# Kernel tuning notes

Measured on AMD Instinct MI355X. Metric: run time of the kernel, lower is better.

## Reference

```python
import jax, jax.numpy as jnp
import numpy as np

N = 20000
E = 320000
D = 512
H = 512


def _gcn_norm(edge_index, num_nodes):
    # PyG GCNConv: add self-loops, then sym-normalize with in-degree of A+I
    src = jnp.concatenate([edge_index[0], jnp.arange(num_nodes)])
    dst = jnp.concatenate([edge_index[1], jnp.arange(num_nodes)])
    deg = jax.ops.segment_sum(jnp.ones_like(dst, dtype=jnp.float32), dst, num_segments=num_nodes)
    dinv = jnp.where(deg > 0, jax.lax.rsqrt(deg), 0.0)
    norm = dinv[src] * dinv[dst]  # [E+N]
    return src, dst, norm


def _gcn_layer(x, src, dst, norm, W, b, num_nodes):
    h = x @ W                          # [N, out]
    msg = h[src] * norm[:, None]       # gather + scale, [E+N, out]
    out = jax.ops.segment_sum(msg, dst, num_segments=num_nodes)  # scatter-add
    return out + b


def setup_inputs() -> dict:
    key = jax.random.key(0)
    ks = jax.random.split(key, 8)
    features = jax.random.normal(ks[0], (N, D), dtype=jnp.float32)
    edge_index = jax.random.randint(ks[1], (2, E), 0, N, dtype=jnp.int64)
    edge_attr = jax.random.normal(ks[2], (E, 1), dtype=jnp.float32)  # unused by GCNConv
    s1 = 1.0 / np.sqrt(D)
    s2 = 1.0 / np.sqrt(H)
    W1 = jax.random.uniform(ks[3], (D, H), dtype=jnp.float32, minval=-s1, maxval=s1)
    b1 = jnp.zeros((H,), dtype=jnp.float32)
    W2 = jax.random.uniform(ks[4], (H, H), dtype=jnp.float32, minval=-s2, maxval=s2)
    b2 = jnp.zeros((H,), dtype=jnp.float32)
    return {"features": features, "edge_index": edge_index, "edge_attr": edge_attr,
            "W1": W1, "b1": b1, "W2": W2, "b2": b2}


def reference(features, edge_index, edge_attr, W1, b1, W2, b2):
    src, dst, norm = _gcn_norm(edge_index, N)
    x = jax.nn.relu(_gcn_layer(features, src, dst, norm, W1, b1, N))
    x = jax.nn.relu(_gcn_layer(x, src, dst, norm, W2, b2, N))
    # global_max_pool over the single graph (batch = all zeros) -> [1, H]
    return jnp.max(x, axis=0, keepdims=True)
```

## Files before the change

### kernel.cpp

```cpp
#include <hip/hip_runtime.h>

#define N_NODES 20000
#define MP      20096
#define N_EDGES 320000
#define DIM     512
#define SCAN_BLOCKS 79
#define FILL_BLOCKS 1250
#define CVT_BLOCKS  2512
#define W_BLOCKS    512
#define SORT_BLOCKS 79
#define NBIN 4096
#define MAXP_BLOCKS 256
#define MAXP_ROWS   79

typedef _Float16 half8 __attribute__((ext_vector_type(8)));
typedef _Float16 half4v __attribute__((ext_vector_type(4)));
typedef float floatx4 __attribute__((ext_vector_type(4)));

#define GLD16(g, l) __builtin_amdgcn_global_load_lds( \
    (const __attribute__((address_space(1))) unsigned int*)(g), \
    (__attribute__((address_space(3))) unsigned int*)(l), 16, 0, 0)

__global__ void k_count(const int* __restrict__ dst, int* __restrict__ cnt) {
    int e = blockIdx.x * blockDim.x + threadIdx.x;
    if (e < N_EDGES) atomicAdd(&cnt[dst[e]], 1);
}

__global__ __launch_bounds__(256) void k_scan_a(const int* __restrict__ cnt,
                                                int* __restrict__ bsum) {
    __shared__ int buf[256];
    int gi = blockIdx.x * 256 + threadIdx.x;
    buf[threadIdx.x] = (gi < N_NODES) ? cnt[gi] : 0;
    __syncthreads();
    for (int off = 128; off > 0; off >>= 1) {
        if (threadIdx.x < off) buf[threadIdx.x] += buf[threadIdx.x + off];
        __syncthreads();
    }
    if (threadIdx.x == 0) bsum[blockIdx.x] = buf[0];
}

__global__ __launch_bounds__(128) void k_scan_b(const int* __restrict__ bsum,
                                                int* __restrict__ bbase) {
    __shared__ int buf[128];
    int tid = threadIdx.x;
    int v = (tid < SCAN_BLOCKS) ? bsum[tid] : 0;
    buf[tid] = v;
    __syncthreads();
    for (int off = 1; off < 128; off <<= 1) {
        int t = (tid >= off) ? buf[tid - off] : 0;
        __syncthreads();
        buf[tid] += t;
        __syncthreads();
    }
    if (tid < SCAN_BLOCKS) bbase[tid] = buf[tid] - v;
}

__global__ __launch_bounds__(256) void k_scan_c(const int* __restrict__ cnt,
                                                const int* __restrict__ bbase,
                                                int* __restrict__ offs,
                                                int* __restrict__ cursor,
                                                float* __restrict__ dinv,
                                                int* __restrict__ hist) {
    __shared__ int buf[256];
    __shared__ int lh[NBIN];
    int tid = threadIdx.x;
#pragma unroll
    for (int k = 0; k < NBIN / 256; ++k) lh[tid + k * 256] = 0;
    int gi = blockIdx.x * 256 + tid;
    int v = (gi < N_NODES) ? cnt[gi] : 0;
    buf[tid] = v;
    __syncthreads();
    for (int off = 1; off < 256; off <<= 1) {
        int t = (tid >= off) ? buf[tid - off] : 0;
        __syncthreads();
        buf[tid] += t;
        __syncthreads();
    }
    int base = bbase[blockIdx.x];
    if (gi < N_NODES) {
        int incl = base + buf[tid];
        offs[gi + 1] = incl;
        cursor[gi] = incl - v;
        dinv[gi] = rsqrtf((float)v + 1.0f);
        if (gi == 0) offs[0] = 0;
        int bin = (v > 255 ? 255 : v) * 16 + (gi & 15);
        atomicAdd(&lh[bin], 1);
    } else if (gi < MP) {
        dinv[gi] = 0.f;
    }
    __syncthreads();
#pragma unroll
    for (int k = 0; k < NBIN / 256; ++k) {
        int b2 = tid + k * 256;
        if (lh[b2]) atomicAdd(&hist[b2], lh[b2]);
    }
}

__global__ __launch_bounds__(256) void k_prep(const int* __restrict__ src,
                                              const int* __restrict__ dst,
                                              int* __restrict__ cursor,
                                              int* __restrict__ csr_src,
                                              const float* __restrict__ F,
                                              _Float16* __restrict__ A,
                                              const float* __restrict__ W1,
                                              const float* __restrict__ W2,
                                              _Float16* __restrict__ Wt1,
                                              _Float16* __restrict__ Wt2,
                                              const int* __restrict__ cnt,
                                              const int* __restrict__ hist,
                                              int* __restrict__ bincur,
                                              int* __restrict__ sorted) {
    int b = blockIdx.x;
    if (b < FILL_BLOCKS) {
        int e = b * 256 + threadIdx.x;
        int d = dst[e];
        int pos = atomicAdd(&cursor[d], 1);
        csr_src[pos] = src[e];
        return;
    }
    if (b < FILL_BLOCKS + CVT_BLOCKS) {
        int base = (b - FILL_BLOCKS) * 1024 + threadIdx.x;
#pragma unroll
        for (int k = 0; k < 4; ++k) {
            int i = base + k * 256;
            int e = i * 4;
            int row = e >> 9;
            half4v o;
            if (row < N_NODES) {
                float4 v = *(const float4*)&F[e];
                o[0] = (_Float16)v.x; o[1] = (_Float16)v.y;
                o[2] = (_Float16)v.z; o[3] = (_Float16)v.w;
            } else {
                o[0] = o[1] = o[2] = o[3] = (_Float16)0.f;
            }
            *(half4v*)&A[e] = o;
        }
        return;
    }
    if (b < FILL_BLOCKS + CVT_BLOCKS + W_BLOCKS) {
        int local = b - (FILL_BLOCKS + CVT_BLOCKS);
        int z = local >> 8, t = local & 255;
        const float* W = z ? W2 : W1;
        _Float16* Wt = z ? Wt2 : Wt1;
        __shared__ float tile[32][33];
        int bx = (t & 15) * 32, by = (t >> 4) * 32;
        int x = threadIdx.x & 31, y4 = (threadIdx.x >> 5) * 4;
#pragma unroll
        for (int r = 0; r < 4; ++r)
            tile[y4 + r][x] = W[(size_t)(by + y4 + r) * DIM + bx + x];
        __syncthreads();
#pragma unroll
        for (int r = 0; r < 4; ++r)
            Wt[(size_t)(bx + y4 + r) * DIM + by + x] = (_Float16)tile[x][y4 + r];
        return;
    }
    int sb = b - (FILL_BLOCKS + CVT_BLOCKS + W_BLOCKS);
    __shared__ int sc[NBIN];
    __shared__ int ps[256];
    int tid = threadIdx.x;
    int tsum = 0;
#pragma unroll
    for (int k = 0; k < NBIN / 256; ++k) {
        int h = hist[tid * (NBIN / 256) + k];
        sc[tid * (NBIN / 256) + k] = tsum;
        tsum += h;
    }
    ps[tid] = tsum;
    __syncthreads();
    for (int off = 1; off < 256; off <<= 1) {
        int t = (tid >= off) ? ps[tid - off] : 0;
        __syncthreads();
        ps[tid] += t;
        __syncthreads();
    }
    int gbase = ps[tid] - tsum;
#pragma unroll
    for (int k = 0; k < NBIN / 256; ++k) sc[tid * (NBIN / 256) + k] += gbase;
    __syncthreads();
    int gi = sb * 256 + tid;
    if (gi < N_NODES) {
        int d = cnt[gi];
        int bin = (d > 255 ? 255 : d) * 16 + (gi & 15);
        int pos = sc[bin] + atomicAdd(&bincur[bin], 1);
        sorted[pos] = gi;
    } else if (gi < MP) {
        sorted[gi] = gi;
    }
}

__global__ __launch_bounds__(256) void k_gemm_f16(const _Float16* __restrict__ A,
                                                  const _Float16* __restrict__ Bt,
                                                  const float* __restrict__ dinv,
                                                  _Float16* __restrict__ G) {
    __shared__ _Float16 As[128 * 32];
    __shared__ _Float16 Bs[128 * 32];

    int t = threadIdx.x;
    int w = t >> 6, lane = t & 63;
    int lm = lane & 15, quad = lane >> 4;
    int m0 = blockIdx.x * 128, n0 = blockIdx.y * 128;
    int wm = (w & 1) * 64, wn = (w >> 1) * 64;

    floatx4 acc[4][4];
#pragma unroll
    for (int i = 0; i < 4; ++i)
#pragma unroll
        for (int j = 0; j < 4; ++j) acc[i][j] = (floatx4){0.f, 0.f, 0.f, 0.f};

    for (int k0 = 0; k0 < DIM; k0 += 32) {
        __syncthreads();
#pragma unroll
        for (int i = 0; i < 2; ++i) {
            int s = i * 256 + t;
            int m = s >> 2, kk = (s & 3) * 8;
            GLD16(A + (size_t)(m0 + m) * DIM + k0 + kk, As + s * 8);
            GLD16(Bt + (size_t)(n0 + m) * DIM + k0 + kk, Bs + s * 8);
        }
        __syncthreads();

        half8 af[4], bf[4];
#pragma unroll
        for (int i = 0; i < 4; ++i)
            af[i] = *(const half8*)&As[(wm + i * 16 + lm) * 32 + quad * 8];
#pragma unroll
        for (int j = 0; j < 4; ++j)
            bf[j] = *(const half8*)&Bs[(wn + j * 16 + lm) * 32 + quad * 8];
#pragma unroll
        for (int i = 0; i < 4; ++i)
#pragma unroll
            for (int j = 0; j < 4; ++j)
                acc[i][j] = __builtin_amdgcn_mfma_f32_16x16x32_f16(af[i], bf[j], acc[i][j], 0, 0, 0);
    }

#pragma unroll
    for (int i = 0; i < 4; ++i)
#pragma unroll
        for (int r = 0; r < 4; ++r) {
            int row = m0 + wm + i * 16 + quad * 4 + r;
            float dd = dinv[row];
#pragma unroll
            for (int j = 0; j < 4; ++j) {
                int col = n0 + wn + j * 16 + lm;
                G[(size_t)row * DIM + col] = (_Float16)(dd * acc[i][j][r]);
            }
        }
}

__global__ __launch_bounds__(256) void k_agg_s(const _Float16* __restrict__ g,
                                               const float* __restrict__ dinv,
                                               const int* __restrict__ offs,
                                               const int* __restrict__ csr_src,
                                               const int* __restrict__ sorted,
                                               const float* __restrict__ bias,
                                               _Float16* __restrict__ out) {
    int chunk = blockIdx.x & 7;
    int grp = blockIdx.x >> 3;
    int w = threadIdx.x >> 6, lane = threadIdx.x & 63;
    int slot = lane >> 3, fg = lane & 7;
    int idx = grp * 32 + w * 8 + slot;
    int node = sorted[idx];
    if ((unsigned)node >= (unsigned)MP) return;
    int fbase = chunk * 64 + fg * 8;
    size_t obase = (size_t)node * DIM + fbase;

    if (node >= N_NODES) {
        half8 z;
#pragma unroll
        for (int i = 0; i < 8; ++i) z[i] = (_Float16)0.f;
        *(half8*)&out[obase] = z;
        return;
    }

    float acc[8];
    half8 self = *(const half8*)&g[obase];
#pragma unroll
    for (int i = 0; i < 8; ++i) acc[i] = (float)self[i];

    int beg = offs[node], end = offs[node + 1];
    int e = beg;
    for (; e + 8 <= end; e += 8) {
        int s0 = csr_src[e],     s1 = csr_src[e + 1], s2 = csr_src[e + 2], s3 = csr_src[e + 3];
        int s4 = csr_src[e + 4], s5 = csr_src[e + 5], s6 = csr_src[e + 6], s7 = csr_src[e + 7];
        half8 v0 = *(const half8*)&g[(size_t)s0 * DIM + fbase];
        half8 v1 = *(const half8*)&g[(size_t)s1 * DIM + fbase];
        half8 v2 = *(const half8*)&g[(size_t)s2 * DIM + fbase];
        half8 v3 = *(const half8*)&g[(size_t)s3 * DIM + fbase];
        half8 v4 = *(const half8*)&g[(size_t)s4 * DIM + fbase];
        half8 v5 = *(const half8*)&g[(size_t)s5 * DIM + fbase];
        half8 v6 = *(const half8*)&g[(size_t)s6 * DIM + fbase];
        half8 v7 = *(const half8*)&g[(size_t)s7 * DIM + fbase];
#pragma unroll
        for (int i = 0; i < 8; ++i)
            acc[i] += (((float)v0[i] + (float)v1[i]) + ((float)v2[i] + (float)v3[i])) +
                      (((float)v4[i] + (float)v5[i]) + ((float)v6[i] + (float)v7[i]));
    }
    for (; e + 4 <= end; e += 4) {
        int s0 = csr_src[e], s1 = csr_src[e + 1], s2 = csr_src[e + 2], s3 = csr_src[e + 3];
        half8 v0 = *(const half8*)&g[(size_t)s0 * DIM + fbase];
        half8 v1 = *(const half8*)&g[(size_t)s1 * DIM + fbase];
        half8 v2 = *(const half8*)&g[(size_t)s2 * DIM + fbase];
        half8 v3 = *(const half8*)&g[(size_t)s3 * DIM + fbase];
#pragma unroll
        for (int i = 0; i < 8; ++i)
            acc[i] += ((float)v0[i] + (float)v1[i]) + ((float)v2[i] + (float)v3[i]);
    }
    for (; e < end; ++e) {
        int s = csr_src[e];
        half8 v = *(const half8*)&g[(size_t)s * DIM + fbase];
#pragma unroll
        for (int i = 0; i < 8; ++i) acc[i] += (float)v[i];
    }

    float dd = dinv[node];
    float4 b0 = *(const float4*)&bias[fbase];
    float4 b1 = *(const float4*)&bias[fbase + 4];
    float bb[8] = {b0.x, b0.y, b0.z, b0.w, b1.x, b1.y, b1.z, b1.w};
    half8 o;
#pragma unroll
    for (int i = 0; i < 8; ++i) o[i] = (_Float16)fmaxf(fmaf(dd, acc[i], bb[i]), 0.f);
    *(half8*)&out[obase] = o;
}

__global__ __launch_bounds__(256) void k_maxpool(const _Float16* __restrict__ x,
                                                 float* __restrict__ out) {
    __shared__ float lmax[4][DIM];
    int stream = threadIdx.x >> 6, lane = threadIdx.x & 63;
    int f0 = lane * 8;
    int r0 = blockIdx.x * MAXP_ROWS;
    int r1 = min(r0 + MAXP_ROWS, N_NODES);

    float m[8];
#pragma unroll
    for (int i = 0; i < 8; ++i) m[i] = 0.f;
    for (int r = r0 + stream; r < r1; r += 4) {
        half8 v = *(const half8*)&x[(size_t)r * DIM + f0];
#pragma unroll
        for (int i = 0; i < 8; ++i) m[i] = fmaxf(m[i], (float)v[i]);
    }
#pragma unroll
    for (int i = 0; i < 8; ++i) lmax[stream][f0 + i] = m[i];
    __syncthreads();
#pragma unroll
    for (int rep = 0; rep < 2; ++rep) {
        int f = rep * 256 + threadIdx.x;
        float v = fmaxf(fmaxf(lmax[0][f], lmax[1][f]), fmaxf(lmax[2][f], lmax[3][f]));
        atomicMax((int*)&out[f], __float_as_int(v));
    }
}

extern "C" void kernel_launch(void* const* d_in, const int* in_sizes, int n_in,
                              void* d_out, int out_size, void* d_ws, size_t ws_size,
                              hipStream_t stream) {
    const float* features = (const float*)d_in[0];
    const int*   ei       = (const int*)d_in[1];
    const float* W1       = (const float*)d_in[3];
    const float* b1       = (const float*)d_in[4];
    const float* W2       = (const float*)d_in[5];
    const float* b2       = (const float*)d_in[6];
    float* out = (float*)d_out;

    const int* src = ei;
    const int* dst = ei + N_EDGES;

    char* p = (char*)d_ws;
    auto alloc = [&](size_t bytes) { void* r = p; p += (bytes + 255) & ~(size_t)255; return r; };
    int*      cnt    = (int*)alloc(N_NODES * 4);
    int*      hist   = (int*)alloc(NBIN * 4);
    int*      bincur = (int*)alloc(NBIN * 4);
    char*     zeroEnd = p;
    int*      offs   = (int*)alloc((N_NODES + 1) * 4);
    int*      cursor = (int*)alloc(N_NODES * 4);
    float*    dinv   = (float*)alloc(MP * 4);
    int*      csr    = (int*)alloc(N_EDGES * 4);
    int*      bsum   = (int*)alloc(SCAN_BLOCKS * 4);
    int*      bbase  = (int*)alloc(SCAN_BLOCKS * 4);
    int*      sorted = (int*)alloc(MP * 4);
    _Float16* fA   = (_Float16*)alloc((size_t)MP * DIM * 2);
    _Float16* Wt1  = (_Float16*)alloc((size_t)DIM * DIM * 2);
    _Float16* Wt2  = (_Float16*)alloc((size_t)DIM * DIM * 2);
    _Float16* gbuf = (_Float16*)alloc((size_t)MP * DIM * 2);
    _Float16* x1f  = (_Float16*)alloc((size_t)MP * DIM * 2);
    _Float16* x2h  = (_Float16*)alloc((size_t)MP * DIM * 2);

    hipMemsetAsync(cnt, 0, (size_t)(zeroEnd - (char*)cnt), stream);
    hipMemsetAsync(out, 0, DIM * 4, stream);

    k_count<<<FILL_BLOCKS, 256, 0, stream>>>(dst, cnt);
    k_scan_a<<<SCAN_BLOCKS, 256, 0, stream>>>(cnt, bsum);
    k_scan_b<<<1, 128, 0, stream>>>(bsum, bbase);
    k_scan_c<<<SCAN_BLOCKS, 256, 0, stream>>>(cnt, bbase, offs, cursor, dinv, hist);

    k_prep<<<FILL_BLOCKS + CVT_BLOCKS + W_BLOCKS + SORT_BLOCKS, 256, 0, stream>>>(
        src, dst, cursor, csr, features, fA, W1, W2, Wt1, Wt2, cnt, hist, bincur, sorted);

    dim3 ggrd(MP / 128, DIM / 128);

    k_gemm_f16<<<ggrd, 256, 0, stream>>>(fA, Wt1, dinv, gbuf);
    k_agg_s<<<8 * (MP / 32), 256, 0, stream>>>(gbuf, dinv, offs, csr, sorted, b1, x1f);

    k_gemm_f16<<<ggrd, 256, 0, stream>>>(x1f, Wt2, dinv, gbuf);
    k_agg_s<<<8 * (MP / 32), 256, 0, stream>>>(gbuf, dinv, offs, csr, sorted, b2, x2h);

    k_maxpool<<<MAXP_BLOCKS, 256, 0, stream>>>(x2h, out);
}
```

Measured before the change: 263.8 us.

## Fuse fp32-to-fp16 feature conversion into first GEMM A-tile load

```diff
diff --git a/kernel.cpp b/kernel.cpp
--- a/kernel.cpp
+++ b/kernel.cpp
@@ -6,7 +6,6 @@
 #define DIM     512
 #define SCAN_BLOCKS 79
 #define FILL_BLOCKS 1250
-#define CVT_BLOCKS  2512
 #define W_BLOCKS    512
 #define SORT_BLOCKS 79
 #define NBIN 4096
@@ -14,12 +13,22 @@
 #define MAXP_ROWS   79
 
 typedef _Float16 half8 __attribute__((ext_vector_type(8)));
-typedef _Float16 half4v __attribute__((ext_vector_type(4)));
 typedef float floatx4 __attribute__((ext_vector_type(4)));
 
 #define GLD16(g, l) __builtin_amdgcn_global_load_lds( \
     (const __attribute__((address_space(1))) unsigned int*)(g), \
     (__attribute__((address_space(3))) unsigned int*)(l), 16, 0, 0)
+
+__device__ inline void store8(_Float16* p, const float* v) {
+    half8 o;
+#pragma unroll
+    for (int i = 0; i < 8; ++i) o[i] = (_Float16)v[i];
+    *(half8*)p = o;
+}
+__device__ inline void store8(float* p, const float* v) {
+    *(float4*)&p[0] = make_float4(v[0], v[1], v[2], v[3]);
+    *(float4*)&p[4] = make_float4(v[4], v[5], v[6], v[7]);
+}
 
 __global__ void k_count(const int* __restrict__ dst, int* __restrict__ cnt) {
     int e = blockIdx.x * blockDim.x + threadIdx.x;
@@ -100,8 +109,6 @@
                                               const int* __restrict__ dst,
                                               int* __restrict__ cursor,
                                               int* __restrict__ csr_src,
-                                              const float* __restrict__ F,
-                                              _Float16* __restrict__ A,
                                               const float* __restrict__ W1,
                                               const float* __restrict__ W2,
                                               _Float16* __restrict__ Wt1,
@@ -118,27 +125,8 @@
         csr_src[pos] = src[e];
         return;
     }
-    if (b < FILL_BLOCKS + CVT_BLOCKS) {
-        int base = (b - FILL_BLOCKS) * 1024 + threadIdx.x;
-#pragma unroll
-        for (int k = 0; k < 4; ++k) {
-            int i = base + k * 256;
-            int e = i * 4;
-            int row = e >> 9;
-            half4v o;
-            if (row < N_NODES) {
-                float4 v = *(const float4*)&F[e];
-                o[0] = (_Float16)v.x; o[1] = (_Float16)v.y;
-                o[2] = (_Float16)v.z; o[3] = (_Float16)v.w;
-            } else {
-                o[0] = o[1] = o[2] = o[3] = (_Float16)0.f;
-            }
-            *(half4v*)&A[e] = o;
-        }
-        return;
-    }
-    if (b < FILL_BLOCKS + CVT_BLOCKS + W_BLOCKS) {
-        int local = b - (FILL_BLOCKS + CVT_BLOCKS);
+    if (b < FILL_BLOCKS + W_BLOCKS) {
+        int local = b - FILL_BLOCKS;
         int z = local >> 8, t = local & 255;
         const float* W = z ? W2 : W1;
         _Float16* Wt = z ? Wt2 : Wt1;
@@ -154,7 +142,7 @@
             Wt[(size_t)(bx + y4 + r) * DIM + by + x] = (_Float16)tile[x][y4 + r];
         return;
     }
-    int sb = b - (FILL_BLOCKS + CVT_BLOCKS + W_BLOCKS);
+    int sb = b - (FILL_BLOCKS + W_BLOCKS);
     __shared__ int sc[NBIN];
     __shared__ int ps[256];
     int tid = threadIdx.x;
@@ -246,13 +234,90 @@
         }
 }
 
-__global__ __launch_bounds__(256) void k_agg_s(const _Float16* __restrict__ g,
+__global__ __launch_bounds__(256) void k_gemm_f32A(const float* __restrict__ A,
+                                                   const _Float16* __restrict__ Bt,
+                                                   const float* __restrict__ dinv,
+                                                   _Float16* __restrict__ G) {
+    __shared__ _Float16 As[128 * 32];
+    __shared__ _Float16 Bs[128 * 32];
+
+    int t = threadIdx.x;
+    int w = t >> 6, lane = t & 63;
+    int lm = lane & 15, quad = lane >> 4;
+    int m0 = blockIdx.x * 128, n0 = blockIdx.y * 128;
+    int wm = (w & 1) * 64, wn = (w >> 1) * 64;
+
+    floatx4 acc[4][4];
+#pragma unroll
+    for (int i = 0; i < 4; ++i)
+#pragma unroll
+        for (int j = 0; j < 4; ++j) acc[i][j] = (floatx4){0.f, 0.f, 0.f, 0.f};
+
+    for (int k0 = 0; k0 < DIM; k0 += 32) {
+        __syncthreads();
+#pragma unroll
+        for (int i = 0; i < 2; ++i) {
+            int s = i * 256 + t;
+            int m = s >> 2, kk = (s & 3) * 8;
+            GLD16(Bt + (size_t)(n0 + m) * DIM + k0 + kk, Bs + s * 8);
+        }
+#pragma unroll
+        for (int i = 0; i < 2; ++i) {
+            int s = i * 256 + t;
+            int m = s >> 2, kk = (s & 3) * 8;
+            int arow = m0 + m;
+            half8 h;
+            if (arow < N_NODES) {
+                float4 a0 = *(const float4*)&A[(size_t)arow * DIM + k0 + kk];
+                float4 a1 = *(const float4*)&A[(size_t)arow * DIM + k0 + kk + 4];
+                h[0] = (_Float16)a0.x; h[1] = (_Float16)a0.y;
+                h[2] = (_Float16)a0.z; h[3] = (_Float16)a0.w;
+                h[4] = (_Float16)a1.x; h[5] = (_Float16)a1.y;
+                h[6] = (_Float16)a1.z; h[7] = (_Float16)a1.w;
+            } else {
+#pragma unroll
+                for (int q = 0; q < 8; ++q) h[q] = (_Float16)0.f;
+            }
+            *(half8*)&As[s * 8] = h;
+        }
+        __syncthreads();
+
+        half8 af[4], bf[4];
+#pragma unroll
+        for (int i = 0; i < 4; ++i)
+            af[i] = *(const half8*)&As[(wm + i * 16 + lm) * 32 + quad * 8];
+#pragma unroll
+        for (int j = 0; j < 4; ++j)
+            bf[j] = *(const half8*)&Bs[(wn + j * 16 + lm) * 32 + quad * 8];
+#pragma unroll
+        for (int i = 0; i < 4; ++i)
+#pragma unroll
+            for (int j = 0; j < 4; ++j)
+                acc[i][j] = __builtin_amdgcn_mfma_f32_16x16x32_f16(af[i], bf[j], acc[i][j], 0, 0, 0);
+    }
+
+#pragma unroll
+    for (int i = 0; i < 4; ++i)
+#pragma unroll
+        for (int r = 0; r < 4; ++r) {
+            int row = m0 + wm + i * 16 + quad * 4 + r;
+            float dd = dinv[row];
+#pragma unroll
+            for (int j = 0; j < 4; ++j) {
+                int col = n0 + wn + j * 16 + lm;
+                G[(size_t)row * DIM + col] = (_Float16)(dd * acc[i][j][r]);
+            }
+        }
+}
+
+template <typename OutT>
+__global__ __launch_bounds__(256) void k_agg_t(const _Float16* __restrict__ g,
                                                const float* __restrict__ dinv,
                                                const int* __restrict__ offs,
                                                const int* __restrict__ csr_src,
                                                const int* __restrict__ sorted,
                                                const float* __restrict__ bias,
-                                               _Float16* __restrict__ out) {
+                                               OutT* __restrict__ out) {
     int chunk = blockIdx.x & 7;
     int grp = blockIdx.x >> 3;
     int w = threadIdx.x >> 6, lane = threadIdx.x & 63;
@@ -264,10 +329,8 @@
     size_t obase = (size_t)node * DIM + fbase;
 
     if (node >= N_NODES) {
-        half8 z;
-#pragma unroll
-        for (int i = 0; i < 8; ++i) z[i] = (_Float16)0.f;
-        *(half8*)&out[obase] = z;
+        float z[8] = {0.f, 0.f, 0.f, 0.f, 0.f, 0.f, 0.f, 0.f};
+        store8(&out[obase], z);
         return;
     }
 
@@ -315,13 +378,13 @@
     float4 b0 = *(const float4*)&bias[fbase];
     float4 b1 = *(const float4*)&bias[fbase + 4];
     float bb[8] = {b0.x, b0.y, b0.z, b0.w, b1.x, b1.y, b1.z, b1.w};
-    half8 o;
-#pragma unroll
-    for (int i = 0; i < 8; ++i) o[i] = (_Float16)fmaxf(fmaf(dd, acc[i], bb[i]), 0.f);
-    *(half8*)&out[obase] = o;
-}
-
-__global__ __launch_bounds__(256) void k_maxpool(const _Float16* __restrict__ x,
+    float o[8];
+#pragma unroll
+    for (int i = 0; i < 8; ++i) o[i] = fmaxf(fmaf(dd, acc[i], bb[i]), 0.f);
+    store8(&out[obase], o);
+}
+
+__global__ __launch_bounds__(256) void k_maxpool(const float* __restrict__ x,
                                                  float* __restrict__ out) {
     __shared__ float lmax[4][DIM];
     int stream = threadIdx.x >> 6, lane = threadIdx.x & 63;
@@ -333,9 +396,12 @@
 #pragma unroll
     for (int i = 0; i < 8; ++i) m[i] = 0.f;
     for (int r = r0 + stream; r < r1; r += 4) {
-        half8 v = *(const half8*)&x[(size_t)r * DIM + f0];
-#pragma unroll
-        for (int i = 0; i < 8; ++i) m[i] = fmaxf(m[i], (float)v[i]);
+        float4 a = *(const float4*)&x[(size_t)r * DIM + f0];
+        float4 b = *(const float4*)&x[(size_t)r * DIM + f0 + 4];
+        m[0] = fmaxf(m[0], a.x); m[1] = fmaxf(m[1], a.y);
+        m[2] = fmaxf(m[2], a.z); m[3] = fmaxf(m[3], a.w);
+        m[4] = fmaxf(m[4], b.x); m[5] = fmaxf(m[5], b.y);
+        m[6] = fmaxf(m[6], b.z); m[7] = fmaxf(m[7], b.w);
     }
 #pragma unroll
     for (int i = 0; i < 8; ++i) lmax[stream][f0 + i] = m[i];
@@ -375,12 +441,11 @@
     int*      bsum   = (int*)alloc(SCAN_BLOCKS * 4);
     int*      bbase  = (int*)alloc(SCAN_BLOCKS * 4);
     int*      sorted = (int*)alloc(MP * 4);
-    _Float16* fA   = (_Float16*)alloc((size_t)MP * DIM * 2);
     _Float16* Wt1  = (_Float16*)alloc((size_t)DIM * DIM * 2);
     _Float16* Wt2  = (_Float16*)alloc((size_t)DIM * DIM * 2);
     _Float16* gbuf = (_Float16*)alloc((size_t)MP * DIM * 2);
     _Float16* x1f  = (_Float16*)alloc((size_t)MP * DIM * 2);
-    _Float16* x2h  = (_Float16*)alloc((size_t)MP * DIM * 2);
+    float*    x2f  = (float*)alloc((size_t)MP * DIM * 4);
 
     hipMemsetAsync(cnt, 0, (size_t)(zeroEnd - (char*)cnt), stream);
     hipMemsetAsync(out, 0, DIM * 4, stream);
@@ -390,16 +455,16 @@
     k_scan_b<<<1, 128, 0, stream>>>(bsum, bbase);
     k_scan_c<<<SCAN_BLOCKS, 256, 0, stream>>>(cnt, bbase, offs, cursor, dinv, hist);
 
-    k_prep<<<FILL_BLOCKS + CVT_BLOCKS + W_BLOCKS + SORT_BLOCKS, 256, 0, stream>>>(
-        src, dst, cursor, csr, features, fA, W1, W2, Wt1, Wt2, cnt, hist, bincur, sorted);
+    k_prep<<<FILL_BLOCKS + W_BLOCKS + SORT_BLOCKS, 256, 0, stream>>>(
+        src, dst, cursor, csr, W1, W2, Wt1, Wt2, cnt, hist, bincur, sorted);
 
     dim3 ggrd(MP / 128, DIM / 128);
 
-    k_gemm_f16<<<ggrd, 256, 0, stream>>>(fA, Wt1, dinv, gbuf);
-    k_agg_s<<<8 * (MP / 32), 256, 0, stream>>>(gbuf, dinv, offs, csr, sorted, b1, x1f);
+    k_gemm_f32A<<<ggrd, 256, 0, stream>>>(features, Wt1, dinv, gbuf);
+    k_agg_t<_Float16><<<8 * (MP / 32), 256, 0, stream>>>(gbuf, dinv, offs, csr, sorted, b1, x1f);
 
     k_gemm_f16<<<ggrd, 256, 0, stream>>>(x1f, Wt2, dinv, gbuf);
-    k_agg_s<<<8 * (MP / 32), 256, 0, stream>>>(gbuf, dinv, offs, csr, sorted, b2, x2h);
-
-    k_maxpool<<<MAXP_BLOCKS, 256, 0, stream>>>(x2h, out);
-}
+    k_agg_t<float><<<8 * (MP / 32), 256, 0, stream>>>(gbuf, dinv, offs, csr, sorted, b2, x2f);
+
+    k_maxpool<<<MAXP_BLOCKS, 256, 0, stream>>>(x2f, out);
+}
```

Result: slower. 271.7 us (+3.0%).
